# Kernel optimization log

Hardware: AMD Instinct MI355X
Metric: run time of the kernel (lower is better)

Reference implementation:

```python
import jax, jax.numpy as jnp
import numpy as np

EPS = 1e-6     # vnn repo EPS used in VN nonlinearity / batchnorm norm
BN_EPS = 1e-5  # torch BatchNorm default eps
K = 40         # args.n_knn


def knn_idx(x, k):
    # x: (B, 3, N) -> (B, N, k) indices of k nearest neighbors (incl. self)
    inner = -2.0 * jnp.einsum('bdn,bdm->bnm', x, x)
    xx = jnp.sum(x * x, axis=1)  # (B, N)
    neg_dist = -xx[:, :, None] - inner - xx[:, None, :]
    _, idx = jax.lax.top_k(neg_dist, k)
    return idx


def get_graph_feature_cross(x, k):
    # x: (B, 3, N) -> (B, 3, 3, N, k): channels are [nbr - ctr, ctr, cross(nbr, ctr)]
    pts = jnp.transpose(x, (0, 2, 1))  # (B, N, 3)
    idx = knn_idx(x, k)                # (B, N, k)
    nbr = jax.vmap(lambda p, i: p[i])(pts, idx)          # (B, N, k, 3)
    ctr = jnp.broadcast_to(pts[:, :, None, :], nbr.shape)
    cross = jnp.cross(nbr, ctr)
    feat = jnp.stack([nbr - ctr, ctr, cross], axis=3)    # (B, N, k, 3, 3)
    return jnp.transpose(feat, (0, 3, 4, 1, 2))          # (B, C=3, 3vec, N, k)


def vn_bn(x):
    # VNBatchNorm (training-mode batch stats, affine = identity at init)
    # x: (B, C, 3, *rest); normalize the per-vector norm across (B, *rest)
    norm = jnp.sqrt(jnp.sum(x * x, axis=2)) + EPS  # (B, C, *rest)
    axes = (0,) + tuple(range(2, norm.ndim))
    mean = jnp.mean(norm, axis=axes, keepdims=True)
    var = jnp.var(norm, axis=axes, keepdims=True)
    norm_bn = (norm - mean) / jnp.sqrt(var + BN_EPS)
    return x / jnp.expand_dims(norm, 2) * jnp.expand_dims(norm_bn, 2)


def vn_lin(W, x):
    # channel-wise linear on axis 1 of (B, C, 3, ...)
    return jnp.einsum('oc,bc...->bo...', W, x)


def vn_lrelu(x, Wf, Wd):
    # VNLinearLeakyReLU with negative_slope=0.0
    p = vn_bn(vn_lin(Wf, x))
    d = vn_lin(Wd, x)
    dot = jnp.sum(p * d, axis=2, keepdims=True)
    dsq = jnp.sum(d * d, axis=2, keepdims=True)
    neg = p - (dot / (dsq + EPS)) * d  # project out the d component
    return jnp.where(dot >= 0, p, neg)


def vn_max_pool(x, W):
    # pool over last axis, picking the element maximizing <x, d> per (B, C, n)
    d = vn_lin(W, x)
    dot = jnp.sum(x * d, axis=2, keepdims=True)          # (B, C, 1, ..., K)
    idx = jnp.argmax(dot, axis=-1, keepdims=True)        # (B, C, 1, ..., 1)
    idx = jnp.broadcast_to(idx, x.shape[:-1] + (1,))
    return jnp.take_along_axis(x, idx, axis=-1)[..., 0]


def setup_inputs() -> dict:
    key = jax.random.key(0)
    ks = jax.random.split(key, 16)
    def w(k, o, i):
        bound = 1.0 / np.sqrt(i)  # torch nn.Linear default init
        return jax.random.uniform(k, (o, i), jnp.float32, -bound, bound)
    B, N = 8, 2048
    C1, C2, C3 = 64 // 3, 128 // 3, 1024 // 3  # 21, 42, 341
    F1, F2 = 512 // 3, 256 // 3                # 170, 85
    return {
        'x': jax.random.normal(ks[0], (B, 3, N), jnp.float32),
        'W_pos_feat': w(ks[1], C1, 3), 'W_pos_dir': w(ks[2], C1, 3),
        'W_gpool': w(ks[3], C1, C1),
        'W1_feat': w(ks[4], C1, C1), 'W1_dir': w(ks[5], C1, C1),
        'W2_feat': w(ks[6], C2, C1), 'W2_dir': w(ks[7], C2, C1),
        'W3_feat': w(ks[8], C3, C2), 'W3_dir': w(ks[9], C3, C2),
        'W_pool': w(ks[10], C3, C3),
        'Wf1_feat': w(ks[11], F1, C3), 'Wf1_dir': w(ks[12], F1, C3),
        'Wf2_feat': w(ks[13], F2, F1), 'Wf2_dir': w(ks[14], F2, F1),
        'Wf3': w(ks[15], 3, F2),
    }


def reference(x, W_pos_feat, W_pos_dir, W_gpool, W1_feat, W1_dir, W2_feat, W2_dir,
              W3_feat, W3_dir, W_pool, Wf1_feat, Wf1_dir, Wf2_feat, Wf2_dir, Wf3):
    feat = get_graph_feature_cross(x, K)            # (B, 3, 3, N, K)
    h = vn_lrelu(feat, W_pos_feat, W_pos_dir)       # (B, 21, 3, N, K)
    h = vn_max_pool(h, W_gpool)                     # (B, 21, 3, N)
    h = vn_lrelu(h, W1_feat, W1_dir)                # (B, 21, 3, N)
    h = vn_lrelu(h, W2_feat, W2_dir)                # (B, 42, 3, N)
    h = vn_lrelu(h, W3_feat, W3_dir)                # (B, 341, 3, N)
    h = vn_max_pool(h, W_pool)                      # (B, 341, 3)
    h = vn_lrelu(h, Wf1_feat, Wf1_dir)              # (B, 170, 3)
    h = vn_lrelu(h, Wf2_feat, Wf2_dir)              # (B, 85, 3)
    return vn_lin(Wf3, h)                           # (B, 3, 3)
```

## Files before the change

kernel.cpp:

```cpp
#include <hip/hip_runtime.h>

#define NP 2048
#define BATCH 8
#define KNN 40
#define EPSF 1e-6f
#define BNEPS 1e-5f

typedef __attribute__((ext_vector_type(8))) short short8;
typedef __attribute__((ext_vector_type(4))) float f32x4;

__device__ __forceinline__ unsigned ordf(float v){
  unsigned u = __float_as_uint(v);
  return (u & 0x80000000u) ? ~u : (u | 0x80000000u);
}

__device__ __forceinline__ void bsplit(float v, unsigned short &h, unsigned short &l){
  unsigned u = __float_as_uint(v);
  unsigned hu = (u + 0x7fffu + ((u >> 16) & 1u)) >> 16;
  h = (unsigned short)hu;
  float r = v - __uint_as_float(hu << 16);
  unsigned u2 = __float_as_uint(r);
  l = (unsigned short)((u2 + 0x7fffu + ((u2 >> 16) & 1u)) >> 16);
}

__device__ __forceinline__ float bf2f(unsigned short h){
  return __uint_as_float(((unsigned)h) << 16);
}

__global__ __launch_bounds__(256) void knn_kernel(const float* __restrict__ x, int* __restrict__ idx){
  __shared__ float4 sP[NP];
  int tid = threadIdx.x;
  int w = tid >> 6, lane = tid & 63;
  int row0 = blockIdx.x * 8 + w * 2, row1 = row0 + 1;
  int b = row0 >> 11;
  int i0 = row0 & 2047, i1 = row1 & 2047;
  const float* xb = x + b * 3 * NP;
  for (int t = tid; t < NP; t += 256){
    float a = xb[t], c = xb[NP + t], d = xb[2*NP + t];
    float xx = __fadd_rn(__fadd_rn(__fmul_rn(a,a), __fmul_rn(c,c)), __fmul_rn(d,d));
    sP[t] = make_float4(a, c, d, xx);
  }
  __syncthreads();
  float4 pa = sP[i0];
  float4 pb = sP[i1];
  const float4* lp = &sP[lane];
  unsigned long long a0 = 0, a1 = 0, a2 = 0, a3 = 0;
  unsigned long long b0 = 0, b1 = 0, b2 = 0, b3 = 0;
  #pragma unroll
  for (int m = 0; m < 32; m++){
    float4 pj = lp[m * 64];
    unsigned lowbits = (unsigned)(2047 - (m*64 + lane));
    float dotA = __fadd_rn(__fadd_rn(__fmul_rn(pa.x, pj.x), __fmul_rn(pa.y, pj.y)), __fmul_rn(pa.z, pj.z));
    float vA = __fsub_rn(__fsub_rn(-pa.w, __fmul_rn(-2.f, dotA)), pj.w);
    unsigned long long pkA = ((unsigned long long)ordf(vA) << 32) | lowbits;
    if (pkA > a3){
      if (pkA > a2){ a3 = a2; if (pkA > a1){ a2 = a1; if (pkA > a0){ a1 = a0; a0 = pkA; } else a1 = pkA; } else a2 = pkA; }
      else a3 = pkA;
    }
    float dotB = __fadd_rn(__fadd_rn(__fmul_rn(pb.x, pj.x), __fmul_rn(pb.y, pj.y)), __fmul_rn(pb.z, pj.z));
    float vB = __fsub_rn(__fsub_rn(-pb.w, __fmul_rn(-2.f, dotB)), pj.w);
    unsigned long long pkB = ((unsigned long long)ordf(vB) << 32) | lowbits;
    if (pkB > b3){
      if (pkB > b2){ b3 = b2; if (pkB > b1){ b2 = b1; if (pkB > b0){ b1 = b0; b0 = pkB; } else b1 = pkB; } else b2 = pkB; }
      else b3 = pkB;
    }
  }
  unsigned outA = 0, outB = 0;
  unsigned long long lastA = ~0ull, lastB = ~0ull;
  for (int kk = 0; kk < KNN; kk++){
    unsigned hvA = (unsigned)(a0 >> 32), hvB = (unsigned)(b0 >> 32);
    unsigned vmA = hvA, vmB = hvB;
    #pragma unroll
    for (int st = 32; st > 0; st >>= 1){
      unsigned oA = (unsigned)__shfl_xor((int)vmA, st, 64);
      unsigned oB = (unsigned)__shfl_xor((int)vmB, st, 64);
      vmA = (oA > vmA) ? oA : vmA;
      vmB = (oB > vmB) ? oB : vmB;
    }
    bool cA = (hvA == vmA), cB = (hvB == vmB);
    unsigned long long mA = __ballot(cA), mB = __ballot(cB);
    unsigned loA, loB;
    if (__popcll(mA) == 1){
      int wl = __ffsll((unsigned long long)mA) - 1;
      loA = (unsigned)__shfl((int)(unsigned)a0, wl, 64);
    } else {
      unsigned cl = cA ? (unsigned)a0 : 0u;
      #pragma unroll
      for (int st = 32; st > 0; st >>= 1){
        unsigned o = (unsigned)__shfl_xor((int)cl, st, 64);
        cl = (o > cl) ? o : cl;
      }
      loA = cl;
    }
    if (__popcll(mB) == 1){
      int wl = __ffsll((unsigned long long)mB) - 1;
      loB = (unsigned)__shfl((int)(unsigned)b0, wl, 64);
    } else {
      unsigned cl = cB ? (unsigned)b0 : 0u;
      #pragma unroll
      for (int st = 32; st > 0; st >>= 1){
        unsigned o = (unsigned)__shfl_xor((int)cl, st, 64);
        cl = (o > cl) ? o : cl;
      }
      loB = cl;
    }
    if (lane == kk){ outA = loA; outB = loB; }
    if (cA && (unsigned)a0 == loA){
      lastA = a0;
      a0 = a1; a1 = a2; a2 = a3; a3 = 0;
      if (a0 == 0){
        unsigned long long best = 0;
        #pragma unroll
        for (int m = 0; m < 32; m++){
          float4 pj = lp[m * 64];
          float dot = __fadd_rn(__fadd_rn(__fmul_rn(pa.x, pj.x), __fmul_rn(pa.y, pj.y)), __fmul_rn(pa.z, pj.z));
          float vv = __fsub_rn(__fsub_rn(-pa.w, __fmul_rn(-2.f, dot)), pj.w);
          unsigned long long pk = ((unsigned long long)ordf(vv) << 32) | (unsigned)(2047 - (m*64 + lane));
          if (pk < lastA && pk > best) best = pk;
        }
        a0 = best;
      }
    }
    if (cB && (unsigned)b0 == loB){
      lastB = b0;
      b0 = b1; b1 = b2; b2 = b3; b3 = 0;
      if (b0 == 0){
        unsigned long long best = 0;
        #pragma unroll
        for (int m = 0; m < 32; m++){
          float4 pj = lp[m * 64];
          float dot = __fadd_rn(__fadd_rn(__fmul_rn(pb.x, pj.x), __fmul_rn(pb.y, pj.y)), __fmul_rn(pb.z, pj.z));
          float vv = __fsub_rn(__fsub_rn(-pb.w, __fmul_rn(-2.f, dot)), pj.w);
          unsigned long long pk = ((unsigned long long)ordf(vv) << 32) | (unsigned)(2047 - (m*64 + lane));
          if (pk < lastB && pk > best) best = pk;
        }
        b0 = best;
      }
    }
  }
  if (lane < KNN){
    idx[row0 * KNN + lane] = 2047 - (int)outA;
    idx[row1 * KNN + lane] = 2047 - (int)outB;
  }
}

__global__ __launch_bounds__(256) void gf_stats(const float* __restrict__ x, const int* __restrict__ idx,
                                                const float* __restrict__ Wf, double* __restrict__ sums){
  int tid0 = blockIdx.x * 256 + threadIdx.x;
  float s[21], q[21];
  #pragma unroll
  for (int o = 0; o < 21; o++){ s[o] = 0.f; q[o] = 0.f; }
  for (int pix = tid0; pix < BATCH * NP * KNN; pix += 256 * 256){
    int rem = pix / KNN;
    int n = rem & 2047, b = rem >> 11;
    int j = idx[pix];
    const float* xb = x + b * 3 * NP;
    float c0 = xb[n], c1 = xb[NP + n], c2 = xb[2*NP + n];
    float a0 = xb[j], a1 = xb[NP + j], a2 = xb[2*NP + j];
    float r0 = a0 - c0, r1 = a1 - c1, r2 = a2 - c2;
    float g0 = a1*c2 - a2*c1, g1 = a2*c0 - a0*c2, g2 = a0*c1 - a1*c0;
    #pragma unroll
    for (int o = 0; o < 21; o++){
      float w0 = Wf[o*3], w1 = Wf[o*3+1], w2 = Wf[o*3+2];
      float p0 = w0*r0 + w1*c0 + w2*g0;
      float p1 = w0*r1 + w1*c1 + w2*g1;
      float p2 = w0*r2 + w1*c2 + w2*g2;
      float nm = sqrtf(p0*p0 + p1*p1 + p2*p2) + EPSF;
      s[o] += nm; q[o] += nm * nm;
    }
  }
  __shared__ float bs[4][42];
  int w = threadIdx.x >> 6;
  #pragma unroll
  for (int o = 0; o < 21; o++){
    float a = s[o], bb = q[o];
    #pragma unroll
    for (int st = 1; st < 64; st <<= 1){ a += __shfl_xor(a, st, 64); bb += __shfl_xor(bb, st, 64); }
    if ((threadIdx.x & 63) == 0){ bs[w][o] = a; bs[w][21 + o] = bb; }
  }
  __syncthreads();
  if (threadIdx.x < 42){
    float tot = bs[0][threadIdx.x] + bs[1][threadIdx.x] + bs[2][threadIdx.x] + bs[3][threadIdx.x];
    int o = threadIdx.x % 21, sq = threadIdx.x / 21;
    atomicAdd(&sums[2*o + sq], (double)tot);
  }
}

__global__ __launch_bounds__(320) void gf_applypool3(const float* __restrict__ x, const int* __restrict__ idx,
    const float* __restrict__ Wf, const float* __restrict__ Wd, const float* __restrict__ Wg,
    const float* __restrict__ mi, float* __restrict__ h1){
  __shared__ unsigned long long sM[8*21];
  const int tid = threadIdx.x;
  for (int t = tid; t < 168; t += 320) sM[t] = 0ull;
  __syncthreads();
  const int pxl = tid / 40, k = tid - pxl * 40;
  const int px = blockIdx.x * 8 + pxl;
  const int b = px >> 11, n = px & 2047;
  const float* xb = x + b * 3 * NP;
  float c0 = xb[n], c1 = xb[NP + n], c2 = xb[2*NP + n];
  int j = idx[(size_t)px * KNN + k];
  float a0 = xb[j], a1 = xb[NP + j], a2 = xb[2*NP + j];
  float r0 = a0 - c0, r1 = a1 - c1, r2 = a2 - c2;
  float g0 = a1*c2 - a2*c1, g1 = a2*c0 - a0*c2, g2 = a0*c1 - a1*c0;
  float h[21][3];
  #pragma unroll
  for (int o = 0; o < 21; o++){
    float w0 = Wf[o*3], w1 = Wf[o*3+1], w2 = Wf[o*3+2];
    float p0 = w0*r0 + w1*c0 + w2*g0;
    float p1 = w0*r1 + w1*c1 + w2*g1;
    float p2 = w0*r2 + w1*c2 + w2*g2;
    float nm = sqrtf(p0*p0 + p1*p1 + p2*p2) + EPSF;
    float f = (nm - mi[2*o]) * mi[2*o+1] / nm;
    p0 *= f; p1 *= f; p2 *= f;
    float v0 = Wd[o*3], v1 = Wd[o*3+1], v2 = Wd[o*3+2];
    float d0 = v0*r0 + v1*c0 + v2*g0;
    float d1 = v0*r1 + v1*c1 + v2*g1;
    float d2 = v0*r2 + v1*c2 + v2*g2;
    float dot = p0*d0 + p1*d1 + p2*d2;
    float dsq = d0*d0 + d1*d1 + d2*d2;
    float t = dot / (dsq + EPSF);
    h[o][0] = (dot >= 0.f) ? p0 : fmaf(-t, d0, p0);
    h[o][1] = (dot >= 0.f) ? p1 : fmaf(-t, d1, p1);
    h[o][2] = (dot >= 0.f) ? p2 : fmaf(-t, d2, p2);
  }
  #pragma unroll
  for (int o = 0; o < 21; o++){
    float q0 = 0.f, q1 = 0.f, q2 = 0.f;
    #pragma unroll
    for (int c = 0; c < 21; c++){
      float wg = Wg[o*21 + c];
      q0 = fmaf(wg, h[c][0], q0); q1 = fmaf(wg, h[c][1], q1); q2 = fmaf(wg, h[c][2], q2);
    }
    float dp = q0*h[o][0] + q1*h[o][1] + q2*h[o][2];
    unsigned long long pk = ((unsigned long long)ordf(dp) << 32) | (unsigned)(63 - k);
    atomicMax(&sM[pxl*21 + o], pk);
  }
  __syncthreads();
  const unsigned mytag = (unsigned)(63 - k);
  #pragma unroll
  for (int o = 0; o < 21; o++){
    if ((unsigned)(sM[pxl*21 + o] & 0xffffffffu) == mytag){
      float* dst = h1 + (size_t)((b*21 + o)*3) * NP + n;
      dst[0] = h[o][0]; dst[NP] = h[o][1]; dst[2*NP] = h[o][2];
    }
  }
}

template<int CIN>
__global__ __launch_bounds__(256) void layer_stats2(const float* __restrict__ hin, const float* __restrict__ Wf,
                                                    double* __restrict__ sums, int Co){
  const int px0 = blockIdx.x * 1024;
  const int b = px0 >> 11;
  const int n0 = (px0 & 2047) + (threadIdx.x << 2);
  const int o0 = blockIdx.y * 8;
  const float* hb = hin + (size_t)b * CIN * 3 * NP + n0;
  float p[8][3][4];
  #pragma unroll
  for (int oo = 0; oo < 8; oo++)
    #pragma unroll
    for (int e = 0; e < 3; e++)
      #pragma unroll
      for (int k = 0; k < 4; k++) p[oo][e][k] = 0.f;
  for (int c = 0; c < CIN; c++){
    float4 hv[3];
    #pragma unroll
    for (int e = 0; e < 3; e++) hv[e] = *(const float4*)&hb[(size_t)(c*3 + e) * NP];
    #pragma unroll
    for (int oo = 0; oo < 8; oo++){
      int o = o0 + oo; if (o >= Co) o = Co - 1;
      float wv = Wf[o*CIN + c];
      #pragma unroll
      for (int e = 0; e < 3; e++){
        p[oo][e][0] = fmaf(wv, hv[e].x, p[oo][e][0]);
        p[oo][e][1] = fmaf(wv, hv[e].y, p[oo][e][1]);
        p[oo][e][2] = fmaf(wv, hv[e].z, p[oo][e][2]);
        p[oo][e][3] = fmaf(wv, hv[e].w, p[oo][e][3]);
      }
    }
  }
  float sl[8], ql[8];
  #pragma unroll
  for (int oo = 0; oo < 8; oo++){
    sl[oo] = 0.f; ql[oo] = 0.f;
    #pragma unroll
    for (int k = 0; k < 4; k++){
      float nm = sqrtf(p[oo][0][k]*p[oo][0][k] + p[oo][1][k]*p[oo][1][k] + p[oo][2][k]*p[oo][2][k]) + EPSF;
      sl[oo] += nm; ql[oo] += nm * nm;
    }
  }
  __shared__ float red[4][16];
  int w = threadIdx.x >> 6;
  #pragma unroll
  for (int oo = 0; oo < 8; oo++){
    float sv = sl[oo], qv = ql[oo];
    #pragma unroll
    for (int st = 1; st < 64; st <<= 1){ sv += __shfl_xor(sv, st, 64); qv += __shfl_xor(qv, st, 64); }
    if ((threadIdx.x & 63) == 0){ red[w][oo] = sv; red[w][8 + oo] = qv; }
  }
  __syncthreads();
  if (threadIdx.x < 16){
    float tot = red[0][threadIdx.x] + red[1][threadIdx.x] + red[2][threadIdx.x] + red[3][threadIdx.x];
    int oo = threadIdx.x & 7, isq = threadIdx.x >> 3;
    int o = o0 + oo;
    if (o < Co) atomicAdd(&sums[2*o + isq], (double)tot);
  }
}

template<int CIN>
__global__ __launch_bounds__(256) void layer_apply2(const float* __restrict__ hin, const float* __restrict__ Wf,
    const float* __restrict__ Wd, const float* __restrict__ mi, float* __restrict__ hout, int Co){
  const int px = blockIdx.x * 256 + threadIdx.x;
  const int b = px >> 11, n = px & 2047;
  const int o0 = blockIdx.y * 8;
  const float* hb = hin + (size_t)b * CIN * 3 * NP + n;
  float p[8][3], d[8][3];
  #pragma unroll
  for (int oo = 0; oo < 8; oo++)
    #pragma unroll
    for (int e = 0; e < 3; e++){ p[oo][e] = 0.f; d[oo][e] = 0.f; }
  for (int c = 0; c < CIN; c++){
    float h0 = hb[(size_t)(c*3 + 0) * NP];
    float h1 = hb[(size_t)(c*3 + 1) * NP];
    float h2 = hb[(size_t)(c*3 + 2) * NP];
    #pragma unroll
    for (int oo = 0; oo < 8; oo++){
      int o = o0 + oo; if (o >= Co) o = Co - 1;
      float wf = Wf[o*CIN + c], wd = Wd[o*CIN + c];
      p[oo][0] = fmaf(wf, h0, p[oo][0]); p[oo][1] = fmaf(wf, h1, p[oo][1]); p[oo][2] = fmaf(wf, h2, p[oo][2]);
      d[oo][0] = fmaf(wd, h0, d[oo][0]); d[oo][1] = fmaf(wd, h1, d[oo][1]); d[oo][2] = fmaf(wd, h2, d[oo][2]);
    }
  }
  #pragma unroll
  for (int oo = 0; oo < 8; oo++){
    int o = o0 + oo;
    if (o < Co){
      float nm = sqrtf(p[oo][0]*p[oo][0] + p[oo][1]*p[oo][1] + p[oo][2]*p[oo][2]) + EPSF;
      float f = (nm - mi[2*o]) * mi[2*o+1] / nm;
      float p0 = p[oo][0]*f, p1 = p[oo][1]*f, p2 = p[oo][2]*f;
      float dot = p0*d[oo][0] + p1*d[oo][1] + p2*d[oo][2];
      float dsq = d[oo][0]*d[oo][0] + d[oo][1]*d[oo][1] + d[oo][2]*d[oo][2];
      float t = dot / (dsq + EPSF);
      float r0 = (dot >= 0.f) ? p0 : fmaf(-t, d[oo][0], p0);
      float r1 = (dot >= 0.f) ? p1 : fmaf(-t, d[oo][1], p1);
      float r2 = (dot >= 0.f) ? p2 : fmaf(-t, d[oo][2], p2);
      float* dst = hout + (size_t)((b*Co + o)*3) * NP + n;
      dst[0] = r0; dst[NP] = r1; dst[2*NP] = r2;
    }
  }
}

__global__ __launch_bounds__(256) void layer_apply2_k(const float* __restrict__ hin, const float* __restrict__ Wf,
    const float* __restrict__ Wd, const float* __restrict__ mi,
    unsigned short* __restrict__ Hk3h, unsigned short* __restrict__ Hk3l){
  const int px = blockIdx.x * 256 + threadIdx.x;
  const int b = px >> 11, n = px & 2047;
  const int kb = blockIdx.y;
  const float* hb = hin + (size_t)b * 21 * 3 * NP + n;
  float r[8][3];
  #pragma unroll
  for (int oo = 0; oo < 8; oo++)
    #pragma unroll
    for (int e = 0; e < 3; e++) r[oo][e] = 0.f;
  if (kb < 6){
    float p[8][3], d[8][3];
    #pragma unroll
    for (int oo = 0; oo < 8; oo++)
      #pragma unroll
      for (int e = 0; e < 3; e++){ p[oo][e] = 0.f; d[oo][e] = 0.f; }
    for (int c = 0; c < 21; c++){
      float h0 = hb[(size_t)(c*3 + 0) * NP];
      float h1 = hb[(size_t)(c*3 + 1) * NP];
      float h2 = hb[(size_t)(c*3 + 2) * NP];
      #pragma unroll
      for (int oo = 0; oo < 8; oo++){
        int o = kb*8 + oo; if (o >= 42) o = 41;
        float wf = Wf[o*21 + c], wd = Wd[o*21 + c];
        p[oo][0] = fmaf(wf, h0, p[oo][0]); p[oo][1] = fmaf(wf, h1, p[oo][1]); p[oo][2] = fmaf(wf, h2, p[oo][2]);
        d[oo][0] = fmaf(wd, h0, d[oo][0]); d[oo][1] = fmaf(wd, h1, d[oo][1]); d[oo][2] = fmaf(wd, h2, d[oo][2]);
      }
    }
    #pragma unroll
    for (int oo = 0; oo < 8; oo++){
      int o = kb*8 + oo;
      if (o < 42){
        float nm = sqrtf(p[oo][0]*p[oo][0] + p[oo][1]*p[oo][1] + p[oo][2]*p[oo][2]) + EPSF;
        float f = (nm - mi[2*o]) * mi[2*o+1] / nm;
        float p0 = p[oo][0]*f, p1 = p[oo][1]*f, p2 = p[oo][2]*f;
        float dot = p0*d[oo][0] + p1*d[oo][1] + p2*d[oo][2];
        float dsq = d[oo][0]*d[oo][0] + d[oo][1]*d[oo][1] + d[oo][2]*d[oo][2];
        float t = dot / (dsq + EPSF);
        r[oo][0] = (dot >= 0.f) ? p0 : fmaf(-t, d[oo][0], p0);
        r[oo][1] = (dot >= 0.f) ? p1 : fmaf(-t, d[oo][1], p1);
        r[oo][2] = (dot >= 0.f) ? p2 : fmaf(-t, d[oo][2], p2);
      }
    }
  }
  #pragma unroll
  for (int e = 0; e < 3; e++){
    unsigned ph[4], pl[4];
    #pragma unroll
    for (int oo = 0; oo < 8; oo++){
      unsigned short hh, ll;
      bsplit(r[oo][e], hh, ll);
      if (!(oo & 1)){ ph[oo>>1] = hh; pl[oo>>1] = ll; }
      else { ph[oo>>1] |= ((unsigned)hh) << 16; pl[oo>>1] |= ((unsigned)ll) << 16; }
    }
    size_t base = ((((size_t)(b*3 + e))*8 + kb) * 2048 + n) * 8;
    *(uint4*)(Hk3h + base) = make_uint4(ph[0], ph[1], ph[2], ph[3]);
    *(uint4*)(Hk3l + base) = make_uint4(pl[0], pl[1], pl[2], pl[3]);
  }
}

__global__ void finalize_stats(const double* __restrict__ sums, float* __restrict__ mi, int Co, double invM){
  int o = blockIdx.x * 64 + threadIdx.x;
  if (o >= Co) return;
  double m = sums[2*o] * invM;
  double v = sums[2*o+1] * invM - m * m;
  if (v < 0.0) v = 0.0;
  mi[2*o] = (float)m;
  mi[2*o+1] = (float)(1.0 / sqrt(v + (double)BNEPS));
}

__global__ __launch_bounds__(256) void wk_kernel(const float* __restrict__ Wp,
    unsigned short* __restrict__ Wkh, unsigned short* __restrict__ Wkl){
  int t = blockIdx.x * 256 + threadIdx.x;
  if (t >= 44*384*8) return;
  int j = t & 7, o = (t >> 3) % 384, cb = t / (384*8);
  int c = cb*8 + j;
  float v = (c < 341 && o < 341) ? Wp[o*341 + c] : 0.f;
  unsigned short h, l;
  bsplit(v, h, l);
  Wkh[t] = h; Wkl[t] = l;
}

__global__ __launch_bounds__(256) void wk3_kernel(const float* __restrict__ W3f, const float* __restrict__ W3d,
    unsigned short* __restrict__ Wfh, unsigned short* __restrict__ Wfl,
    unsigned short* __restrict__ Wdh, unsigned short* __restrict__ Wdl){
  int t = blockIdx.x * 256 + threadIdx.x;
  if (t >= 8*384*8) return;
  int j = t & 7, o = (t >> 3) % 384, cb = t / (384*8);
  int c = cb*8 + j;
  bool ok = (c < 42 && o < 341);
  float vf = ok ? W3f[o*42 + c] : 0.f;
  float vd = ok ? W3d[o*42 + c] : 0.f;
  unsigned short h, l;
  bsplit(vf, h, l); Wfh[t] = h; Wfl[t] = l;
  bsplit(vd, h, l); Wdh[t] = h; Wdl[t] = l;
}

__global__ __launch_bounds__(256) void stats3_mfma(const unsigned short* __restrict__ Wfh,
    const unsigned short* __restrict__ Wfl, const unsigned short* __restrict__ Hh,
    const unsigned short* __restrict__ Hl, double* __restrict__ sums){
  __shared__ unsigned short sB[2][8][64][8];
  const int b = blockIdx.z, o0 = blockIdx.y * 64, n0 = blockIdx.x * 64;
  const int t = threadIdx.x, w = t >> 6, l = t & 63;
  const int r = l & 15, g = l >> 4;
  const int wo = o0 + w * 16;
  const int skb = t >> 5, sn = (t & 31) * 2;
  f32x4 acc[3][4];
  #pragma unroll
  for (int e = 0; e < 3; e++)
    #pragma unroll
    for (int nt = 0; nt < 4; nt++) acc[e][nt] = (f32x4)0.f;
  for (int e = 0; e < 3; e++){
    if (e) __syncthreads();
    const uint4* srcH = (const uint4*)(Hh + ((((size_t)(b*3 + e))*8 + skb) * 2048 + n0 + sn) * 8);
    const uint4* srcL = (const uint4*)(Hl + ((((size_t)(b*3 + e))*8 + skb) * 2048 + n0 + sn) * 8);
    uint4 h0 = srcH[0], h1 = srcH[1], l0 = srcL[0], l1 = srcL[1];
    *(uint4*)&sB[0][skb][sn][0] = h0; *(uint4*)&sB[0][skb][sn+1][0] = h1;
    *(uint4*)&sB[1][skb][sn][0] = l0; *(uint4*)&sB[1][skb][sn+1][0] = l1;
    __syncthreads();
    #pragma unroll
    for (int kt = 0; kt < 2; kt++){
      size_t aoff = (((size_t)(kt*4 + g)) * 384 + wo + r) * 8;
      short8 ah = *(const short8*)(Wfh + aoff);
      short8 al = *(const short8*)(Wfl + aoff);
      #pragma unroll
      for (int nt = 0; nt < 4; nt++){
        short8 bh = *(const short8*)&sB[0][kt*4 + g][nt*16 + r][0];
        short8 bl = *(const short8*)&sB[1][kt*4 + g][nt*16 + r][0];
        acc[e][nt] = __builtin_amdgcn_mfma_f32_16x16x32_bf16(ah, bh, acc[e][nt], 0, 0, 0);
        acc[e][nt] = __builtin_amdgcn_mfma_f32_16x16x32_bf16(ah, bl, acc[e][nt], 0, 0, 0);
        acc[e][nt] = __builtin_amdgcn_mfma_f32_16x16x32_bf16(al, bh, acc[e][nt], 0, 0, 0);
      }
    }
  }
  #pragma unroll
  for (int jj = 0; jj < 4; jj++){
    int o = wo + g*4 + jj;
    float s1 = 0.f, s2 = 0.f;
    #pragma unroll
    for (int nt = 0; nt < 4; nt++){
      float p0 = acc[0][nt][jj], p1 = acc[1][nt][jj], p2 = acc[2][nt][jj];
      float nm = sqrtf(p0*p0 + p1*p1 + p2*p2) + EPSF;
      s1 += nm; s2 += nm * nm;
    }
    #pragma unroll
    for (int st = 1; st < 16; st <<= 1){
      s1 += __shfl_xor(s1, st, 64);
      s2 += __shfl_xor(s2, st, 64);
    }
    if (r == 0 && o < 341){
      atomicAdd(&sums[2*o], (double)s1);
      atomicAdd(&sums[2*o+1], (double)s2);
    }
  }
}

__global__ __launch_bounds__(256) void apply3_mfma(const unsigned short* __restrict__ Wfh,
    const unsigned short* __restrict__ Wfl, const unsigned short* __restrict__ Wdh,
    const unsigned short* __restrict__ Wdl, const unsigned short* __restrict__ Hh,
    const unsigned short* __restrict__ Hl, const float* __restrict__ mi,
    unsigned short* __restrict__ Hkh, unsigned short* __restrict__ Hkl){
  __shared__ unsigned short sB[2][8][64][8];
  const int b = blockIdx.z, o0 = blockIdx.y * 64, n0 = blockIdx.x * 64;
  const int t = threadIdx.x, w = t >> 6, l = t & 63;
  const int r = l & 15, g = l >> 4;
  const int wo = o0 + w * 16;
  const int skb = t >> 5, sn = (t & 31) * 2;
  f32x4 accp[3][4], accd[3][4];
  #pragma unroll
  for (int e = 0; e < 3; e++)
    #pragma unroll
    for (int nt = 0; nt < 4; nt++){ accp[e][nt] = (f32x4)0.f; accd[e][nt] = (f32x4)0.f; }
  for (int e = 0; e < 3; e++){
    if (e) __syncthreads();
    const uint4* srcH = (const uint4*)(Hh + ((((size_t)(b*3 + e))*8 + skb) * 2048 + n0 + sn) * 8);
    const uint4* srcL = (const uint4*)(Hl + ((((size_t)(b*3 + e))*8 + skb) * 2048 + n0 + sn) * 8);
    uint4 h0 = srcH[0], h1 = srcH[1], l0 = srcL[0], l1 = srcL[1];
    *(uint4*)&sB[0][skb][sn][0] = h0; *(uint4*)&sB[0][skb][sn+1][0] = h1;
    *(uint4*)&sB[1][skb][sn][0] = l0; *(uint4*)&sB[1][skb][sn+1][0] = l1;
    __syncthreads();
    #pragma unroll
    for (int kt = 0; kt < 2; kt++){
      size_t aoff = (((size_t)(kt*4 + g)) * 384 + wo + r) * 8;
      short8 afh = *(const short8*)(Wfh + aoff);
      short8 afl = *(const short8*)(Wfl + aoff);
      short8 adh = *(const short8*)(Wdh + aoff);
      short8 adl = *(const short8*)(Wdl + aoff);
      #pragma unroll
      for (int nt = 0; nt < 4; nt++){
        short8 bh = *(const short8*)&sB[0][kt*4 + g][nt*16 + r][0];
        short8 bl = *(const short8*)&sB[1][kt*4 + g][nt*16 + r][0];
        accp[e][nt] = __builtin_amdgcn_mfma_f32_16x16x32_bf16(afh, bh, accp[e][nt], 0, 0, 0);
        accp[e][nt] = __builtin_amdgcn_mfma_f32_16x16x32_bf16(afh, bl, accp[e][nt], 0, 0, 0);
        accp[e][nt] = __builtin_amdgcn_mfma_f32_16x16x32_bf16(afl, bh, accp[e][nt], 0, 0, 0);
        accd[e][nt] = __builtin_amdgcn_mfma_f32_16x16x32_bf16(adh, bh, accd[e][nt], 0, 0, 0);
        accd[e][nt] = __builtin_amdgcn_mfma_f32_16x16x32_bf16(adh, bl, accd[e][nt], 0, 0, 0);
        accd[e][nt] = __builtin_amdgcn_mfma_f32_16x16x32_bf16(adl, bh, accd[e][nt], 0, 0, 0);
      }
    }
  }
  const int obase = wo + g*4;
  const int kb = obase >> 3, jo = obase & 7;
  #pragma unroll
  for (int nt = 0; nt < 4; nt++){
    float rr[3][4];
    #pragma unroll
    for (int jj = 0; jj < 4; jj++){
      int o = obase + jj;
      float r0 = 0.f, r1 = 0.f, r2 = 0.f;
      if (o < 341){
        float p0 = accp[0][nt][jj], p1 = accp[1][nt][jj], p2 = accp[2][nt][jj];
        float d0 = accd[0][nt][jj], d1 = accd[1][nt][jj], d2 = accd[2][nt][jj];
        float nm = sqrtf(p0*p0 + p1*p1 + p2*p2) + EPSF;
        float f = (nm - mi[2*o]) * mi[2*o+1] / nm;
        p0 *= f; p1 *= f; p2 *= f;
        float dot = p0*d0 + p1*d1 + p2*d2;
        float dsq = d0*d0 + d1*d1 + d2*d2;
        float tt = dot / (dsq + EPSF);
        r0 = (dot >= 0.f) ? p0 : fmaf(-tt, d0, p0);
        r1 = (dot >= 0.f) ? p1 : fmaf(-tt, d1, p1);
        r2 = (dot >= 0.f) ? p2 : fmaf(-tt, d2, p2);
      }
      rr[0][jj] = r0; rr[1][jj] = r1; rr[2][jj] = r2;
    }
    int n = n0 + nt*16 + r;
    #pragma unroll
    for (int e = 0; e < 3; e++){
      unsigned short h0, l0, h1, l1, h2, l2, h3, l3;
      bsplit(rr[e][0], h0, l0); bsplit(rr[e][1], h1, l1);
      bsplit(rr[e][2], h2, l2); bsplit(rr[e][3], h3, l3);
      unsigned ph0 = (unsigned)h0 | ((unsigned)h1 << 16);
      unsigned ph1 = (unsigned)h2 | ((unsigned)h3 << 16);
      unsigned pl0 = (unsigned)l0 | ((unsigned)l1 << 16);
      unsigned pl1 = (unsigned)l2 | ((unsigned)l3 << 16);
      size_t base = ((((size_t)(b*3 + e))*48 + kb) * 2048 + (size_t)n) * 8 + jo;
      *(uint2*)(Hkh + base) = make_uint2(ph0, ph1);
      *(uint2*)(Hkl + base) = make_uint2(pl0, pl1);
    }
  }
}

__global__ __launch_bounds__(256) void pool_mfma(const unsigned short* __restrict__ Wkh,
    const unsigned short* __restrict__ Wkl, const unsigned short* __restrict__ Hkh,
    const unsigned short* __restrict__ Hkl, unsigned long long* __restrict__ packed){
  __shared__ unsigned short sB[2][2][4][64][8];
  const int b = blockIdx.z, o0 = blockIdx.y * 64, n0 = blockIdx.x * 64;
  const int t = threadIdx.x, w = t >> 6, l = t & 63;
  const int wo = o0 + w * 16;
  const int r = l & 15, g = l >> 4;
  const int skb = t >> 6, sn = t & 63;
  const int ktw = wo >> 5;

  f32x4 acc[4], dotv[4], hval[4];
  #pragma unroll
  for (int nt = 0; nt < 4; nt++){ dotv[nt] = (f32x4)0.f; hval[nt] = (f32x4)0.f; }

  auto gsrc = [&](const unsigned short* base, int e, int kt) -> const uint4* {
    return (const uint4*)(base + ((((size_t)(b*3 + e))*48 + (size_t)(kt*4 + skb)) * 2048 + n0 + sn) * 8);
  };

  uint4 rg[2];
  rg[0] = *gsrc(Hkh, 0, 0);
  rg[1] = *gsrc(Hkl, 0, 0);

  for (int ek = 0; ek < 33; ek++){
    const int e = ek / 11, kt = ek - e*11, buf = ek & 1;
    *(uint4*)&sB[buf][0][skb][sn][0] = rg[0];
    *(uint4*)&sB[buf][1][skb][sn][0] = rg[1];
    __syncthreads();
    if (ek < 32){
      int e2 = (ek+1) / 11, kt2 = (ek+1) - e2*11;
      rg[0] = *gsrc(Hkh, e2, kt2);
      rg[1] = *gsrc(Hkl, e2, kt2);
    }
    if (kt == 0){
      #pragma unroll
      for (int nt = 0; nt < 4; nt++) acc[nt] = (f32x4)0.f;
    }
    size_t aoff = (((size_t)(kt*4 + g)) * 384 + (wo + r)) * 8;
    short8 ah = *(const short8*)(Wkh + aoff);
    short8 al = *(const short8*)(Wkl + aoff);
    #pragma unroll
    for (int nt = 0; nt < 4; nt++){
      short8 bh = *(const short8*)&sB[buf][0][g][nt*16 + r][0];
      short8 bl = *(const short8*)&sB[buf][1][g][nt*16 + r][0];
      acc[nt] = __builtin_amdgcn_mfma_f32_16x16x32_bf16(ah, bh, acc[nt], 0, 0, 0);
      acc[nt] = __builtin_amdgcn_mfma_f32_16x16x32_bf16(ah, bl, acc[nt], 0, 0, 0);
      acc[nt] = __builtin_amdgcn_mfma_f32_16x16x32_bf16(al, bh, acc[nt], 0, 0, 0);
    }
    if (kt == ktw){
      #pragma unroll
      for (int jj = 0; jj < 4; jj++){
        int oin = (wo & 31) + g*4 + jj;
        #pragma unroll
        for (int nt = 0; nt < 4; nt++){
          hval[nt][jj] = bf2f(sB[buf][0][oin>>3][nt*16 + r][oin&7])
                       + bf2f(sB[buf][1][oin>>3][nt*16 + r][oin&7]);
        }
      }
    }
    __syncthreads();
    if (kt == 10){
      #pragma unroll
      for (int nt = 0; nt < 4; nt++)
        #pragma unroll
        for (int jj = 0; jj < 4; jj++)
          dotv[nt][jj] += acc[nt][jj] * hval[nt][jj];
    }
  }
  #pragma unroll
  for (int j = 0; j < 4; j++){
    int o = wo + g*4 + j;
    unsigned long long best = 0;
    #pragma unroll
    for (int nt = 0; nt < 4; nt++){
      int n = n0 + nt*16 + r;
      unsigned long long pk = ((unsigned long long)ordf(dotv[nt][j]) << 32) | (unsigned)(2047 - n);
      if (pk > best) best = pk;
    }
    #pragma unroll
    for (int st = 1; st < 16; st <<= 1){
      unsigned long long ob = __shfl_xor(best, st, 64);
      if (ob > best) best = ob;
    }
    if (r == 0 && o < 341) atomicMax(&packed[b*341 + o], best);
  }
}

__global__ void pool_gather(const unsigned long long* __restrict__ packed,
                            const unsigned short* __restrict__ Hkh, const unsigned short* __restrict__ Hkl,
                            float* __restrict__ pooled){
  int t = blockIdx.x * 256 + threadIdx.x;
  if (t >= BATCH * 341) return;
  int n = 2047 - (int)(packed[t] & 0xffffffffu);
  int b = t / 341, o = t % 341;
  #pragma unroll
  for (int e = 0; e < 3; e++){
    size_t hb = ((((size_t)(b*3 + e))*48 + (o >> 3)) * 2048 + n) * 8 + (o & 7);
    pooled[t*3 + e] = bf2f(Hkh[hb]) + bf2f(Hkl[hb]);
  }
}

__global__ __launch_bounds__(64) void flayer(const float* __restrict__ in, const float* __restrict__ Wf,
    const float* __restrict__ Wd, float* __restrict__ out, int Cin, int Co){
  int o = blockIdx.x, lane = threadIdx.x;
  float pv[24], dv[24];
  #pragma unroll
  for (int be = 0; be < 24; be++){ pv[be] = 0.f; dv[be] = 0.f; }
  for (int c = lane; c < Cin; c += 64){
    float wf = Wf[o*Cin + c], wd = Wd[o*Cin + c];
    #pragma unroll
    for (int bb = 0; bb < 8; bb++){
      #pragma unroll
      for (int e = 0; e < 3; e++){
        float hv = in[(bb*Cin + c)*3 + e];
        pv[bb*3+e] = fmaf(wf, hv, pv[bb*3+e]);
        dv[bb*3+e] = fmaf(wd, hv, dv[bb*3+e]);
      }
    }
  }
  #pragma unroll
  for (int be = 0; be < 24; be++){
    #pragma unroll
    for (int st = 1; st < 64; st <<= 1){
      pv[be] += __shfl_xor(pv[be], st, 64);
      dv[be] += __shfl_xor(dv[be], st, 64);
    }
  }
  float nm[8], dotb[8], dsqb[8];
  float mean = 0.f;
  #pragma unroll
  for (int bb = 0; bb < 8; bb++){
    nm[bb] = sqrtf(pv[bb*3]*pv[bb*3] + pv[bb*3+1]*pv[bb*3+1] + pv[bb*3+2]*pv[bb*3+2]) + EPSF;
    mean += nm[bb];
  }
  mean *= 0.125f;
  float var = 0.f;
  #pragma unroll
  for (int bb = 0; bb < 8; bb++){ float dvv = nm[bb] - mean; var += dvv * dvv; }
  var *= 0.125f;
  float istd = 1.f / sqrtf(var + BNEPS);
  #pragma unroll
  for (int bb = 0; bb < 8; bb++){
    float f = (nm[bb] - mean) * istd / nm[bb];
    dotb[bb] = f * (pv[bb*3]*dv[bb*3] + pv[bb*3+1]*dv[bb*3+1] + pv[bb*3+2]*dv[bb*3+2]);
    dsqb[bb] = dv[bb*3]*dv[bb*3] + dv[bb*3+1]*dv[bb*3+1] + dv[bb*3+2]*dv[bb*3+2];
  }
  #pragma unroll
  for (int be = 0; be < 24; be++){
    if (lane == be){
      int bb = be / 3;
      float f = (nm[bb] - mean) * istd / nm[bb];
      float pe = pv[be] * f;
      float t = dotb[bb] / (dsqb[bb] + EPSF);
      float res = (dotb[bb] >= 0.f) ? pe : fmaf(-t, dv[be], pe);
      out[(bb*Co + o)*3 + (be % 3)] = res;
    }
  }
}

__global__ void final_lin(const float* __restrict__ in, const float* __restrict__ W, float* __restrict__ out){
  int t = threadIdx.x;
  if (t >= 72) return;
  int b = t / 9, o = (t % 9) / 3, e = t % 3;
  float s = 0.f;
  for (int c = 0; c < 85; c++) s = fmaf(W[o*85 + c], in[(b*85 + c)*3 + e], s);
  out[t] = s;
}

extern "C" void kernel_launch(void* const* d_in, const int* in_sizes, int n_in,
                              void* d_out, int out_size, void* d_ws, size_t ws_size,
                              hipStream_t stream){
  const float* x   = (const float*)d_in[0];
  const float* Wpf = (const float*)d_in[1];
  const float* Wpd = (const float*)d_in[2];
  const float* Wg  = (const float*)d_in[3];
  const float* W1f = (const float*)d_in[4];
  const float* W1d = (const float*)d_in[5];
  const float* W2f = (const float*)d_in[6];
  const float* W2d = (const float*)d_in[7];
  const float* W3f = (const float*)d_in[8];
  const float* W3d = (const float*)d_in[9];
  const float* Wpool = (const float*)d_in[10];
  const float* Wf1f = (const float*)d_in[11];
  const float* Wf1d = (const float*)d_in[12];
  const float* Wf2f = (const float*)d_in[13];
  const float* Wf2d = (const float*)d_in[14];
  const float* Wf3  = (const float*)d_in[15];
  float* out = (float*)d_out;

  char* ws = (char*)d_ws;
  size_t off = 0;
  int*   idx  = (int*)(ws + off);             off += (size_t)BATCH*NP*KNN*4;
  float* h1  = (float*)(ws + off);            off += (size_t)BATCH*21*3*NP*4;
  float* h2  = (float*)(ws + off);            off += (size_t)BATCH*21*3*NP*4;
  unsigned short* Hk3h = (unsigned short*)(ws + off); off += (size_t)BATCH*3*8*NP*8*2;
  unsigned short* Hk3l = (unsigned short*)(ws + off); off += (size_t)BATCH*3*8*NP*8*2;
  unsigned short* Hkh = (unsigned short*)(ws + off); off += (size_t)BATCH*3*48*NP*8*2;
  unsigned short* Hkl = (unsigned short*)(ws + off); off += (size_t)BATCH*3*48*NP*8*2;
  unsigned short* Wkh = (unsigned short*)(ws + off); off += (size_t)44*384*8*2;
  unsigned short* Wkl = (unsigned short*)(ws + off); off += (size_t)44*384*8*2;
  unsigned short* Wk3fh = (unsigned short*)(ws + off); off += (size_t)8*384*8*2;
  unsigned short* Wk3fl = (unsigned short*)(ws + off); off += (size_t)8*384*8*2;
  unsigned short* Wk3dh = (unsigned short*)(ws + off); off += (size_t)8*384*8*2;
  unsigned short* Wk3dl = (unsigned short*)(ws + off); off += (size_t)8*384*8*2;
  char*  zbase = ws + off;
  double* sums_gf = (double*)(ws + off);      off += 8192;
  double* sums_l1 = (double*)(ws + off);      off += 8192;
  double* sums_l2 = (double*)(ws + off);      off += 8192;
  double* sums_l3 = (double*)(ws + off);      off += 8192;
  unsigned long long* packed = (unsigned long long*)(ws + off); off += 24576;
  size_t zbytes = (ws + off) - zbase;
  float* mi_gf = (float*)(ws + off);          off += 1024;
  float* mi_l1 = (float*)(ws + off);          off += 1024;
  float* mi_l2 = (float*)(ws + off);          off += 1024;
  float* mi_l3 = (float*)(ws + off);          off += 4096;
  float* pooled = (float*)(ws + off);         off += (size_t)BATCH*341*3*4 + 32;
  float* h5 = (float*)(ws + off);             off += (size_t)BATCH*170*3*4 + 32;
  float* h6 = (float*)(ws + off);             off += (size_t)BATCH*85*3*4 + 32;

  hipMemsetAsync(zbase, 0, zbytes, stream);

  knn_kernel<<<BATCH*NP/8, 256, 0, stream>>>(x, idx);
  wk_kernel<<<(44*384*8 + 255)/256, 256, 0, stream>>>(Wpool, Wkh, Wkl);
  wk3_kernel<<<(8*384*8 + 255)/256, 256, 0, stream>>>(W3f, W3d, Wk3fh, Wk3fl, Wk3dh, Wk3dl);

  gf_stats<<<256, 256, 0, stream>>>(x, idx, Wpf, sums_gf);
  finalize_stats<<<1, 64, 0, stream>>>(sums_gf, mi_gf, 21, 1.0 / (double)(BATCH*NP*KNN));
  gf_applypool3<<<BATCH*NP/8, 320, 0, stream>>>(x, idx, Wpf, Wpd, Wg, mi_gf, h1);

  layer_stats2<21><<<dim3(16,3), 256, 0, stream>>>(h1, W1f, sums_l1, 21);
  finalize_stats<<<1, 64, 0, stream>>>(sums_l1, mi_l1, 21, 1.0 / (double)(BATCH*NP));
  layer_apply2<21><<<dim3(64,3), 256, 0, stream>>>(h1, W1f, W1d, mi_l1, h2, 21);

  layer_stats2<21><<<dim3(16,6), 256, 0, stream>>>(h2, W2f, sums_l2, 42);
  finalize_stats<<<1, 64, 0, stream>>>(sums_l2, mi_l2, 42, 1.0 / (double)(BATCH*NP));
  layer_apply2_k<<<dim3(64,8), 256, 0, stream>>>(h2, W2f, W2d, mi_l2, Hk3h, Hk3l);

  stats3_mfma<<<dim3(32, 6, BATCH), 256, 0, stream>>>(Wk3fh, Wk3fl, Hk3h, Hk3l, sums_l3);
  finalize_stats<<<6, 64, 0, stream>>>(sums_l3, mi_l3, 341, 1.0 / (double)(BATCH*NP));
  apply3_mfma<<<dim3(32, 6, BATCH), 256, 0, stream>>>(Wk3fh, Wk3fl, Wk3dh, Wk3dl, Hk3h, Hk3l, mi_l3, Hkh, Hkl);

  pool_mfma<<<dim3(32, 6, BATCH), 256, 0, stream>>>(Wkh, Wkl, Hkh, Hkl, packed);
  pool_gather<<<(BATCH*341 + 255)/256, 256, 0, stream>>>(packed, Hkh, Hkl, pooled);

  flayer<<<170, 64, 0, stream>>>(pooled, Wf1f, Wf1d, h5, 341, 170);
  flayer<<<85, 64, 0, stream>>>(h5, Wf2f, Wf2d, h6, 170, 85);
  final_lin<<<1, 128, 0, stream>>>(h6, Wf3, out);
}
```

Measured before the change: 520.6 us.

## Drop LDS staging in pool_mfma and double output channels per wave

The pooling MFMA kernel no longer stages the H tiles through double-buffered shared memory with barriers. Each wave now reads B fragments straight from global memory and computes 32 output channels instead of 16, so the block tile grows to 128 channels and the grid halves in y. The gating values are read from global memory per channel after each e-slice instead of being picked out of shared memory. This removes the syncthreads and LDS traffic and reuses each B load across two A fragments. In exchange it relies on the cache for B reuse across the four waves, adds scattered 2-byte global loads, and uses more accumulator registers.

After: 543.4 us. 1.04x slower.

```diff
diff --git a/kernel.cpp b/kernel.cpp
--- a/kernel.cpp
+++ b/kernel.cpp
@@ -595,87 +595,79 @@
 __global__ __launch_bounds__(256) void pool_mfma(const unsigned short* __restrict__ Wkh,
     const unsigned short* __restrict__ Wkl, const unsigned short* __restrict__ Hkh,
     const unsigned short* __restrict__ Hkl, unsigned long long* __restrict__ packed){
-  __shared__ unsigned short sB[2][2][4][64][8];
-  const int b = blockIdx.z, o0 = blockIdx.y * 64, n0 = blockIdx.x * 64;
+  const int b = blockIdx.z, o0 = blockIdx.y * 128, n0 = blockIdx.x * 64;
   const int t = threadIdx.x, w = t >> 6, l = t & 63;
-  const int wo = o0 + w * 16;
+  const int wo = o0 + w * 32;
   const int r = l & 15, g = l >> 4;
-  const int skb = t >> 6, sn = t & 63;
-  const int ktw = wo >> 5;
-
-  f32x4 acc[4], dotv[4], hval[4];
-  #pragma unroll
-  for (int nt = 0; nt < 4; nt++){ dotv[nt] = (f32x4)0.f; hval[nt] = (f32x4)0.f; }
-
-  auto gsrc = [&](const unsigned short* base, int e, int kt) -> const uint4* {
-    return (const uint4*)(base + ((((size_t)(b*3 + e))*48 + (size_t)(kt*4 + skb)) * 2048 + n0 + sn) * 8);
-  };
-
-  uint4 rg[2];
-  rg[0] = *gsrc(Hkh, 0, 0);
-  rg[1] = *gsrc(Hkl, 0, 0);
-
-  for (int ek = 0; ek < 33; ek++){
-    const int e = ek / 11, kt = ek - e*11, buf = ek & 1;
-    *(uint4*)&sB[buf][0][skb][sn][0] = rg[0];
-    *(uint4*)&sB[buf][1][skb][sn][0] = rg[1];
-    __syncthreads();
-    if (ek < 32){
-      int e2 = (ek+1) / 11, kt2 = (ek+1) - e2*11;
-      rg[0] = *gsrc(Hkh, e2, kt2);
-      rg[1] = *gsrc(Hkl, e2, kt2);
-    }
-    if (kt == 0){
-      #pragma unroll
-      for (int nt = 0; nt < 4; nt++) acc[nt] = (f32x4)0.f;
-    }
-    size_t aoff = (((size_t)(kt*4 + g)) * 384 + (wo + r)) * 8;
-    short8 ah = *(const short8*)(Wkh + aoff);
-    short8 al = *(const short8*)(Wkl + aoff);
-    #pragma unroll
-    for (int nt = 0; nt < 4; nt++){
-      short8 bh = *(const short8*)&sB[buf][0][g][nt*16 + r][0];
-      short8 bl = *(const short8*)&sB[buf][1][g][nt*16 + r][0];
-      acc[nt] = __builtin_amdgcn_mfma_f32_16x16x32_bf16(ah, bh, acc[nt], 0, 0, 0);
-      acc[nt] = __builtin_amdgcn_mfma_f32_16x16x32_bf16(ah, bl, acc[nt], 0, 0, 0);
-      acc[nt] = __builtin_amdgcn_mfma_f32_16x16x32_bf16(al, bh, acc[nt], 0, 0, 0);
-    }
-    if (kt == ktw){
+
+  f32x4 acc[2][4], dotv[2][4];
+  #pragma unroll
+  for (int s = 0; s < 2; s++)
+    #pragma unroll
+    for (int nt = 0; nt < 4; nt++) dotv[s][nt] = (f32x4)0.f;
+
+  for (int e = 0; e < 3; e++){
+    #pragma unroll
+    for (int s = 0; s < 2; s++)
+      #pragma unroll
+      for (int nt = 0; nt < 4; nt++) acc[s][nt] = (f32x4)0.f;
+    for (int kt = 0; kt < 11; kt++){
+      short8 ah[2], al[2];
+      #pragma unroll
+      for (int s = 0; s < 2; s++){
+        size_t aoff = (((size_t)(kt*4 + g)) * 384 + (wo + s*16 + r)) * 8;
+        ah[s] = *(const short8*)(Wkh + aoff);
+        al[s] = *(const short8*)(Wkl + aoff);
+      }
+      size_t hbase = ((((size_t)(b*3 + e))*48 + (size_t)(kt*4 + g)) * 2048 + n0) * 8;
+      #pragma unroll
+      for (int nt = 0; nt < 4; nt++){
+        short8 bh = *(const short8*)(Hkh + hbase + (size_t)(nt*16 + r) * 8);
+        short8 bl = *(const short8*)(Hkl + hbase + (size_t)(nt*16 + r) * 8);
+        #pragma unroll
+        for (int s = 0; s < 2; s++){
+          acc[s][nt] = __builtin_amdgcn_mfma_f32_16x16x32_bf16(ah[s], bh, acc[s][nt], 0, 0, 0);
+          acc[s][nt] = __builtin_amdgcn_mfma_f32_16x16x32_bf16(ah[s], bl, acc[s][nt], 0, 0, 0);
+          acc[s][nt] = __builtin_amdgcn_mfma_f32_16x16x32_bf16(al[s], bh, acc[s][nt], 0, 0, 0);
+        }
+      }
+    }
+    #pragma unroll
+    for (int s = 0; s < 2; s++){
       #pragma unroll
       for (int jj = 0; jj < 4; jj++){
-        int oin = (wo & 31) + g*4 + jj;
-        #pragma unroll
-        for (int nt = 0; nt < 4; nt++){
-          hval[nt][jj] = bf2f(sB[buf][0][oin>>3][nt*16 + r][oin&7])
-                       + bf2f(sB[buf][1][oin>>3][nt*16 + r][oin&7]);
+        int o = wo + s*16 + g*4 + jj;
+        if (o < 341){
+          size_t hb = ((((size_t)(b*3 + e))*48 + (size_t)(o >> 3)) * 2048) * 8 + (o & 7);
+          #pragma unroll
+          for (int nt = 0; nt < 4; nt++){
+            int n = n0 + nt*16 + r;
+            float v = bf2f(Hkh[hb + (size_t)n*8]) + bf2f(Hkl[hb + (size_t)n*8]);
+            dotv[s][nt][jj] += acc[s][nt][jj] * v;
+          }
         }
       }
     }
-    __syncthreads();
-    if (kt == 10){
-      #pragma unroll
-      for (int nt = 0; nt < 4; nt++)
-        #pragma unroll
-        for (int jj = 0; jj < 4; jj++)
-          dotv[nt][jj] += acc[nt][jj] * hval[nt][jj];
-    }
-  }
-  #pragma unroll
-  for (int j = 0; j < 4; j++){
-    int o = wo + g*4 + j;
-    unsigned long long best = 0;
-    #pragma unroll
-    for (int nt = 0; nt < 4; nt++){
-      int n = n0 + nt*16 + r;
-      unsigned long long pk = ((unsigned long long)ordf(dotv[nt][j]) << 32) | (unsigned)(2047 - n);
-      if (pk > best) best = pk;
-    }
-    #pragma unroll
-    for (int st = 1; st < 16; st <<= 1){
-      unsigned long long ob = __shfl_xor(best, st, 64);
-      if (ob > best) best = ob;
-    }
-    if (r == 0 && o < 341) atomicMax(&packed[b*341 + o], best);
+  }
+  #pragma unroll
+  for (int s = 0; s < 2; s++){
+    #pragma unroll
+    for (int j = 0; j < 4; j++){
+      int o = wo + s*16 + g*4 + j;
+      unsigned long long best = 0;
+      #pragma unroll
+      for (int nt = 0; nt < 4; nt++){
+        int n = n0 + nt*16 + r;
+        unsigned long long pk = ((unsigned long long)ordf(dotv[s][nt][j]) << 32) | (unsigned)(2047 - n);
+        if (pk > best) best = pk;
+      }
+      #pragma unroll
+      for (int st = 1; st < 16; st <<= 1){
+        unsigned long long ob = __shfl_xor(best, st, 64);
+        if (ob > best) best = ob;
+      }
+      if (r == 0 && o < 341) atomicMax(&packed[b*341 + o], best);
+    }
   }
 }
 
@@ -833,7 +825,7 @@
   finalize_stats<<<6, 64, 0, stream>>>(sums_l3, mi_l3, 341, 1.0 / (double)(BATCH*NP));
   apply3_mfma<<<dim3(32, 6, BATCH), 256, 0, stream>>>(Wk3fh, Wk3fl, Wk3dh, Wk3dl, Hk3h, Hk3l, mi_l3, Hkh, Hkl);
 
-  pool_mfma<<<dim3(32, 6, BATCH), 256, 0, stream>>>(Wkh, Wkl, Hkh, Hkl, packed);
+  pool_mfma<<<dim3(32, 3, BATCH), 256, 0, stream>>>(Wkh, Wkl, Hkh, Hkl, packed);
   pool_gather<<<(BATCH*341 + 255)/256, 256, 0, stream>>>(packed, Hkh, Hkl, pooled);
 
   flayer<<<170, 64, 0, stream>>>(pooled, Wf1f, Wf1d, h5, 341, 170);
```
